# Kernel tuning notes

Measured on AMD Instinct MI355X. Metric: run time of the kernel, lower is better.

The kernel has to match this reference:

```python
import jax, jax.numpy as jnp
import numpy as np
from jax import lax

V, E, H, B, S = 100000, 256, 256, 16, 64
NEG = -1e9


def setup_inputs() -> dict:
    key = jax.random.key(0)
    ks = jax.random.split(key, 20)
    sc = 0.05
    inp = {
        "x": jax.random.randint(ks[0], (B, S), 0, V),
        "mask": jax.random.randint(ks[1], (B, S), 0, 2).astype(jnp.int32),
        "TASK": 0,
        # embedding table (pretrained embedding copied into nn.Embedding)
        "embed": jax.random.normal(ks[2], (V, E), jnp.float32) * sc,
        # shared LSTM (torch gate order i,f,g,o)
        "W_ih": jax.random.normal(ks[3], (4 * H, E), jnp.float32) * sc,
        "W_hh": jax.random.normal(ks[4], (4 * H, H), jnp.float32) * sc,
        "b_ih": jax.random.normal(ks[5], (4 * H,), jnp.float32) * sc,
        "b_hh": jax.random.normal(ks[6], (4 * H,), jnp.float32) * sc,
        # task-specific attention: Ws: (E+2H)->H, Us: H->1
        "Ws_w": jax.random.normal(ks[7], (H, E + 2 * H), jnp.float32) * sc,
        "Ws_b": jax.random.normal(ks[8], (H,), jnp.float32) * sc,
        "Us_w": jax.random.normal(ks[9], (1, H), jnp.float32) * sc,
        "Us_b": jax.random.normal(ks[10], (1,), jnp.float32) * sc,
        # message LSTM cell: gates from x_t, h_{t-1}, message Rt
        "Wx": jax.random.normal(ks[11], (4 * H, E), jnp.float32) * sc,
        "Wh": jax.random.normal(ks[12], (4 * H, H), jnp.float32) * sc,
        "Wm": jax.random.normal(ks[13], (4 * H, H), jnp.float32) * sc,
        "b_cell": jax.random.normal(ks[14], (4 * H,), jnp.float32) * sc,
        # final classifier
        "fc_w": jax.random.normal(ks[15], (1, H), jnp.float32) * sc,
        "fc_b": jax.random.normal(ks[16], (1,), jnp.float32) * sc,
    }
    return inp


def _lstm_gates(g, c):
    i, f, gg, o = jnp.split(g, 4, axis=-1)
    c_new = jax.nn.sigmoid(f) * c + jax.nn.sigmoid(i) * jnp.tanh(gg)
    h_new = jax.nn.sigmoid(o) * jnp.tanh(c_new)
    return h_new, c_new


def _forward(x, mask, embed, W_ih, W_hh, b_ih, b_hh, Ws_w, Ws_b, Us_w, Us_b,
             Wx, Wh, Wm, b_cell, fc_w, fc_b):
    b, s = x.shape
    h_dim = W_hh.shape[1]
    emb = embed[x]                              # [B,S,E]
    emb_t = jnp.transpose(emb, (1, 0, 2))       # [S,B,E]
    z = jnp.zeros((b, h_dim), emb.dtype)

    def shared_step(carry, e_t):
        h, c = carry
        g = e_t @ W_ih.T + h @ W_hh.T + (b_ih + b_hh)
        h, c = _lstm_gates(g, c)
        return (h, c), h

    _, shared_t = lax.scan(shared_step, (z, z), emb_t)   # [S,B,H]
    shared = jnp.transpose(shared_t, (1, 0, 2))          # [B,S,H]
    valid = mask != 0                                    # [B,S]

    def task_step(carry, e_t):
        h, c = carry
        h_task = jnp.broadcast_to(h[:, None, :], shared.shape)      # [B,S,H]
        cat = jnp.concatenate([shared, h_task, emb], axis=2)        # [B,S,E+2H]
        var2 = jnp.tanh(cat @ Ws_w.T + Ws_b)                        # [B,S,H]
        Si = (var2 @ Us_w.T + Us_b)[..., 0]                         # [B,S]
        att = jax.nn.softmax(jnp.where(valid, Si, NEG), axis=1)     # masked softmax over S
        Rt = jnp.einsum('bs,bsh->bh', att, shared)                  # [B,H]
        g = e_t @ Wx.T + h @ Wh.T + Rt @ Wm.T + b_cell
        h, c = _lstm_gates(g, c)
        return (h, c), None

    (h_last, _), _ = lax.scan(jax.checkpoint(task_step), (z, z), emb_t)
    return jax.nn.sigmoid(h_last @ fc_w.T + fc_b)        # [B,1]


def reference(x, mask, TASK, embed, W_ih, W_hh, b_ih, b_hh, Ws_w, Ws_b,
              Us_w, Us_b, Wx, Wh, Wm, b_cell, fc_w, fc_b):
    # TASK selects an entry of task_specific_lstm_list, but the list holds the
    # same module object num_tasks times, so one parameter set is used.
    del TASK
    return _forward(x, mask, embed, W_ih, W_hh, b_ih, b_hh, Ws_w, Ws_b,
                    Us_w, Us_b, Wx, Wh, Wm, b_cell, fc_w, fc_b)
```

## Files before the change

### kernel.cpp

```cpp
#include <hip/hip_runtime.h>

#define NEGV -1e9f

#define OFF_X1   0u
#define OFF_XX   1048576u
#define OFF_A    2097152u
#define OFF_SH   2359296u
#define OFF_SWM  2621440u
#define OFF_HX2  3670016u
#define OFF_HX4  3686400u
#define OFF_PSI  3702784u
#define OFF_AT   OFF_X1

__device__ __forceinline__ float sigf(float x) { return 1.f / (1.f + __expf(-x)); }
__device__ __forceinline__ float tanhfast(float x) {
  float e = __expf(2.f * x);
  return 1.f - __fdividef(2.f, e + 1.f);
}

__device__ __forceinline__ unsigned long long gloadU64(const unsigned long long* p) {
  return __hip_atomic_load(p, __ATOMIC_RELAXED, __HIP_MEMORY_SCOPE_AGENT);
}
__device__ __forceinline__ void gstoreU64(unsigned long long* p, unsigned long long v) {
  __hip_atomic_store(p, v, __ATOMIC_RELAXED, __HIP_MEMORY_SCOPE_AGENT);
}

__device__ __forceinline__ void tile_mm(const float* __restrict__ W, int ldw, int wcol0,
                                        int j0, const float* eL, float* wL, float acc[8]) {
  const int i = threadIdx.x >> 4, jj = threadIdx.x & 15;
  for (int kc = 0; kc < 4; ++kc) {
    __syncthreads();
    const int k0 = kc * 64;
    #pragma unroll
    for (int m = 0; m < 32; ++m) {
      int v = threadIdx.x + (m << 8);
      int row = v >> 6, col = v & 63;
      wL[row * 68 + col] = W[(j0 + row) * ldw + wcol0 + k0 + col];
    }
    __syncthreads();
    const float* ebase = eL + i * 260 + k0;
    #pragma unroll 4
    for (int k4 = 0; k4 < 16; ++k4) {
      float4 e4 = *(const float4*)(ebase + k4 * 4);
      #pragma unroll
      for (int u = 0; u < 8; ++u) {
        float4 w4 = *(const float4*)(wL + (jj + (u << 4)) * 68 + k4 * 4);
        acc[u] += e4.x * w4.x + e4.y * w4.y + e4.z * w4.z + e4.w * w4.w;
      }
    }
  }
}

__global__ __launch_bounds__(256) void k1_precompute(
    const int* __restrict__ x, const float* __restrict__ embed,
    const float* __restrict__ W_ih, const float* __restrict__ b_ih,
    const float* __restrict__ b_hh, const float* __restrict__ Ws_w,
    const float* __restrict__ Ws_b, const float* __restrict__ Wx,
    const float* __restrict__ b_cell, float* __restrict__ ws) {
  __shared__ float eL[16 * 260];
  __shared__ float wL[128 * 68];
  const int rt = blockIdx.x / 18, jb = blockIdx.x % 18;
  if (blockIdx.x == 0) {
    for (int i = threadIdx.x; i < 65536; i += 256) ws[OFF_HX2 + i] = 0.f;
  }
  for (int i = 0; i < 16; ++i) {
    int xi = x[rt * 16 + i];
    eL[i * 260 + threadIdx.x] = embed[xi * 256 + threadIdx.x];
  }
  const float* W; const float* bias1; const float* bias2 = nullptr;
  int ldw, wcol0, j0, ostride; float* out;
  if (jb < 8)       { W = W_ih; ldw = 256; wcol0 = 0;   j0 = jb * 128;        out = ws + OFF_X1; ostride = 1024; bias1 = b_ih; bias2 = b_hh; }
  else if (jb < 16) { W = Wx;   ldw = 256; wcol0 = 0;   j0 = (jb - 8) * 128;  out = ws + OFF_XX; ostride = 1024; bias1 = b_cell; }
  else              { W = Ws_w; ldw = 768; wcol0 = 512; j0 = (jb - 16) * 128; out = ws + OFF_A;  ostride = 256;  bias1 = Ws_b; }
  float acc[8];
  #pragma unroll
  for (int u = 0; u < 8; ++u) acc[u] = 0.f;
  tile_mm(W, ldw, wcol0, j0, eL, wL, acc);
  const int i = threadIdx.x >> 4, jj = threadIdx.x & 15;
  const int r = rt * 16 + i;
  #pragma unroll
  for (int u = 0; u < 8; ++u) {
    int j = j0 + jj + (u << 4);
    float bv = bias1[j] + (bias2 ? bias2[j] : 0.f);
    out[r * ostride + j] = acc[u] + bv;
  }
}

__global__ __launch_bounds__(512) void k2_shared_lstm(
    const float* __restrict__ W_hh, float* __restrict__ ws) {
  const int b = blockIdx.x & 15, j = blockIdx.x >> 4;
  const int t = threadIdx.x;
  const int rl = t >> 2, q = t & 3;
  const int grow = ((rl >> 5) << 8) + (j << 5) + (rl & 31);
  __shared__ float x1L[64 * 128];
  __shared__ __align__(16) float hL[256];
  __shared__ float gA[128];
  unsigned long long* hx = (unsigned long long*)(ws + OFF_HX2);
  float* sh = ws + OFF_SH;
  const float* X1 = ws + OFF_X1;

  float4 wv[16];
  {
    const float* wp = W_hh + grow * 256 + (q << 6);
    #pragma unroll
    for (int m = 0; m < 16; ++m) wv[m] = *(const float4*)(wp + 4 * m);
  }
  for (int v = t; v < 8192; v += 512) {
    int st = v >> 7, r = v & 127;
    int col = ((r >> 5) << 8) + (j << 5) + (r & 31);
    x1L[v] = X1[(b * 64 + st) * 1024 + col];
  }
  float c_reg = 0.f;
  __syncthreads();

  for (int st = 0; st < 64; ++st) {
    if (t < 256) {
      const unsigned long long* p = hx + (unsigned)(st & 1) * 4096u + b * 256 + t;
      unsigned long long v = gloadU64(p);
      while ((unsigned)(v >> 32) < (unsigned)st) v = gloadU64(p);
      hL[t] = __uint_as_float((unsigned)v);
    }
    __syncthreads();
    float p = 0.f;
    const float* hp = hL + (q << 6);
    #pragma unroll
    for (int m = 0; m < 16; ++m) {
      float4 h4 = *(const float4*)(hp + 4 * m);
      p += wv[m].x * h4.x + wv[m].y * h4.y + wv[m].z * h4.z + wv[m].w * h4.w;
    }
    p += __shfl_xor(p, 1); p += __shfl_xor(p, 2);
    if (q == 0) gA[rl] = p + x1L[st * 128 + rl];
    __syncthreads();
    if (t < 32) {
      float gi = gA[t], gf = gA[32 + t], gg = gA[64 + t], go = gA[96 + t];
      c_reg = sigf(gf) * c_reg + sigf(gi) * tanhfast(gg);
      float hn = sigf(go) * tanhfast(c_reg);
      sh[(b * 64 + st) * 256 + (j << 5) + t] = hn;
      unsigned long long pv = ((unsigned long long)(unsigned)(st + 1) << 32)
                            | (unsigned long long)__float_as_uint(hn);
      gstoreU64(hx + (unsigned)((st + 1) & 1) * 4096u + b * 256 + (j << 5) + t, pv);
    }
  }
}

__global__ __launch_bounds__(256) void k3_precompute2(
    const float* __restrict__ Ws_w, const float* __restrict__ Wm,
    float* __restrict__ ws) {
  __shared__ float eL[16 * 260];
  __shared__ float wL[128 * 68];
  const int rt = blockIdx.x / 10, jb = blockIdx.x % 10;
  const float* sh = ws + OFF_SH;
  for (int i = 0; i < 16; ++i)
    eL[i * 260 + threadIdx.x] = sh[(rt * 16 + i) * 256 + threadIdx.x];
  const float* W; int ldw, wcol0, j0; bool addmode;
  if (jb < 8) { W = Wm;   ldw = 256; wcol0 = 0; j0 = jb * 128;       addmode = false; }
  else        { W = Ws_w; ldw = 768; wcol0 = 0; j0 = (jb - 8) * 128; addmode = true; }
  float acc[8];
  #pragma unroll
  for (int u = 0; u < 8; ++u) acc[u] = 0.f;
  tile_mm(W, ldw, wcol0, j0, eL, wL, acc);
  const int i = threadIdx.x >> 4, jj = threadIdx.x & 15;
  const int r = rt * 16 + i;
  if (addmode) {
    const float* Aemb = ws + OFF_A;
    float* AT = ws + OFF_AT;
    const int bb = r >> 6, s = r & 63;
    #pragma unroll
    for (int u = 0; u < 8; ++u) {
      int j = j0 + jj + (u << 4);
      AT[bb * 16384 + j * 64 + s] = Aemb[r * 256 + j] + acc[u];
    }
  } else {
    float* out = ws + OFF_SWM;
    #pragma unroll
    for (int u = 0; u < 8; ++u) {
      int j = j0 + jj + (u << 4);
      out[r * 1024 + j] = acc[u];
    }
  }
}

__global__ __launch_bounds__(512) void k4_task_lstm(
    const int* __restrict__ mask, const float* __restrict__ Ws_w,
    const float* __restrict__ Us_w, const float* __restrict__ Wh,
    const float* __restrict__ fc_w, const float* __restrict__ fc_b,
    float* __restrict__ ws, float* __restrict__ out) {
  const int b = blockIdx.x & 15, j = blockIdx.x >> 4;
  const int t = threadIdx.x;
  const int rl = t >> 2, q = t & 3;
  const int grow = ((rl >> 5) << 8) + (j << 5) + (rl & 31);
  const int hwrow = t >> 4, hwc = t & 15;
  const int kq = t >> 6, sl = t & 63;

  __shared__ __align__(16) float swmB[4 * 128 * 20];
  __shared__ __align__(16) float aTo[32 * 65];
  __shared__ __align__(16) float hL[256];
  __shared__ float hwOwn[32];
  __shared__ float usOwn[32];
  __shared__ float part[8 * 64];
  __shared__ float psiA[512];
  __shared__ __align__(16) float attL[64];
  __shared__ float gA[128];
  __shared__ float redL[4];
  __shared__ int   mL[64];

  unsigned long long* hx   = (unsigned long long*)(ws + OFF_HX4);
  unsigned long long* psiX = (unsigned long long*)(ws + OFF_PSI);
  const float* AT  = ws + OFF_AT;
  const float* SWM = ws + OFF_SWM;
  const float* Xx  = ws + OFF_XX;

  float4 w2v[4];
  {
    const float* p2 = Ws_w + (j * 32 + hwrow) * 768 + 256 + (hwc << 4);
    #pragma unroll
    for (int m = 0; m < 4; ++m) w2v[m] = *(const float4*)(p2 + 4 * m);
  }
  float4 whv[16];
  {
    const float* pw = Wh + grow * 256 + (q << 6);
    #pragma unroll
    for (int m = 0; m < 16; ++m) whv[m] = *(const float4*)(pw + 4 * m);
  }
  for (int v = t; v < 2048; v += 512)
    aTo[(v >> 6) * 65 + (v & 63)] = AT[b * 16384 + j * 2048 + v];
  for (int v = t; v < 8192; v += 512) {
    int s = v >> 7, r = v & 127;
    int col = ((r >> 5) << 8) + (j << 5) + (r & 31);
    swmB[(s >> 4) * 2560 + r * 20 + (s & 15)] = SWM[(b * 64 + s) * 1024 + col];
  }
  if (t < 32) usOwn[t] = Us_w[j * 32 + t];
  if (t < 64) mL[t] = mask[b * 64 + t];
  float c_reg = 0.f;
  __syncthreads();

  for (int st = 0; st < 64; ++st) {
    float xx_r = 0.f;
    if (q == 0) xx_r = Xx[(b * 64 + st) * 1024 + grow];
    if (t < 256) {
      const unsigned long long* p = hx + (unsigned)(st & 1) * 4096u + b * 256 + t;
      unsigned long long v = gloadU64(p);
      while ((unsigned)(v >> 32) < (unsigned)st) v = gloadU64(p);
      hL[t] = __uint_as_float((unsigned)v);
    }
    __syncthreads();
    {
      const float* hp = hL + (hwc << 4);
      float p = 0.f;
      #pragma unroll
      for (int m = 0; m < 4; ++m) {
        float4 h4 = *(const float4*)(hp + 4 * m);
        p += w2v[m].x * h4.x + w2v[m].y * h4.y + w2v[m].z * h4.z + w2v[m].w * h4.w;
      }
      p += __shfl_xor(p, 1); p += __shfl_xor(p, 2);
      p += __shfl_xor(p, 4); p += __shfl_xor(p, 8);
      if (hwc == 0) hwOwn[hwrow] = p;
    }
    __syncthreads();
    {
      float ps = 0.f;
      #pragma unroll
      for (int i2 = 0; i2 < 4; ++i2) {
        int kk = (kq << 2) + i2;
        ps += usOwn[kk] * tanhfast(aTo[kk * 65 + sl] + hwOwn[kk]);
      }
      part[(kq << 6) + sl] = ps;
    }
    __syncthreads();
    if (t < 64) {
      float ps = 0.f;
      #pragma unroll
      for (int w = 0; w < 8; ++w) ps += part[(w << 6) + t];
      unsigned long long pv = ((unsigned long long)(unsigned)(st + 1) << 32)
                            | (unsigned long long)__float_as_uint(ps);
      gstoreU64(psiX + ((unsigned)(st & 1) * 16u + b) * 512u + (j << 6) + t, pv);
    }
    float pwh = 0.f;
    {
      const float* hp = hL + (q << 6);
      #pragma unroll
      for (int m = 0; m < 16; ++m) {
        float4 h4 = *(const float4*)(hp + 4 * m);
        pwh += whv[m].x * h4.x + whv[m].y * h4.y + whv[m].z * h4.z + whv[m].w * h4.w;
      }
    }
    {
      const unsigned long long* p = psiX + ((unsigned)(st & 1) * 16u + b) * 512u + t;
      unsigned long long v = gloadU64(p);
      while ((unsigned)(v >> 32) < (unsigned)(st + 1)) v = gloadU64(p);
      psiA[t] = __uint_as_float((unsigned)v);
    }
    __syncthreads();
    if (t < 64) {
      float acc = 0.f;
      #pragma unroll
      for (int w = 0; w < 8; ++w) acc += psiA[(w << 6) + t];
      float v = mL[t] ? acc : NEGV;
      float mx = v;
      #pragma unroll
      for (int d = 1; d < 64; d <<= 1) mx = fmaxf(mx, __shfl_xor(mx, d));
      float e = __expf(v - mx);
      float ssum = e;
      #pragma unroll
      for (int d = 1; d < 64; d <<= 1) ssum += __shfl_xor(ssum, d);
      attL[t] = e / ssum;
    }
    __syncthreads();
    {
      float p = pwh;
      const float* sb = swmB + q * 2560 + rl * 20;
      const float* atb = attL + (q << 4);
      #pragma unroll
      for (int i2 = 0; i2 < 4; ++i2) {
        float4 s4 = *(const float4*)(sb + 4 * i2);
        float4 a4 = *(const float4*)(atb + 4 * i2);
        p += s4.x * a4.x + s4.y * a4.y + s4.z * a4.z + s4.w * a4.w;
      }
      p += __shfl_xor(p, 1); p += __shfl_xor(p, 2);
      if (q == 0) gA[rl] = p + xx_r;
    }
    __syncthreads();
    if (t < 32) {
      float gi = gA[t], gf = gA[32 + t], gg = gA[64 + t], go = gA[96 + t];
      c_reg = sigf(gf) * c_reg + sigf(gi) * tanhfast(gg);
      float hn = sigf(go) * tanhfast(c_reg);
      unsigned long long pv = ((unsigned long long)(unsigned)(st + 1) << 32)
                            | (unsigned long long)__float_as_uint(hn);
      gstoreU64(hx + (unsigned)((st + 1) & 1) * 4096u + b * 256 + (j << 5) + t, pv);
    }
  }

  if (j == 0) {
    float v = 0.f;
    if (t < 256) {
      const unsigned long long* p = hx + 0 * 4096u + b * 256 + t;
      unsigned long long vv = gloadU64(p);
      while ((unsigned)(vv >> 32) < 64u) vv = gloadU64(p);
      v = __uint_as_float((unsigned)vv) * fc_w[t];
    }
    #pragma unroll
    for (int d = 1; d < 64; d <<= 1) v += __shfl_xor(v, d);
    if (t < 256 && (t & 63) == 0) redL[t >> 6] = v;
    __syncthreads();
    if (t == 0) out[b] = sigf(redL[0] + redL[1] + redL[2] + redL[3] + fc_b[0]);
  }
}

extern "C" void kernel_launch(void* const* d_in, const int* in_sizes, int n_in,
                              void* d_out, int out_size, void* d_ws, size_t ws_size,
                              hipStream_t stream) {
  const int*   x      = (const int*)d_in[0];
  const int*   mask   = (const int*)d_in[1];
  const float* embed  = (const float*)d_in[3];
  const float* W_ih   = (const float*)d_in[4];
  const float* W_hh   = (const float*)d_in[5];
  const float* b_ih   = (const float*)d_in[6];
  const float* b_hh   = (const float*)d_in[7];
  const float* Ws_w   = (const float*)d_in[8];
  const float* Ws_b   = (const float*)d_in[9];
  const float* Us_w   = (const float*)d_in[10];
  const float* Wx     = (const float*)d_in[12];
  const float* Wh     = (const float*)d_in[13];
  const float* Wm     = (const float*)d_in[14];
  const float* b_cell = (const float*)d_in[15];
  const float* fc_w   = (const float*)d_in[16];
  const float* fc_b   = (const float*)d_in[17];
  float* ws  = (float*)d_ws;
  float* out = (float*)d_out;

  k1_precompute<<<dim3(1152), dim3(256), 0, stream>>>(
      x, embed, W_ih, b_ih, b_hh, Ws_w, Ws_b, Wx, b_cell, ws);
  k2_shared_lstm<<<dim3(128), dim3(512), 0, stream>>>(W_hh, ws);
  k3_precompute2<<<dim3(640), dim3(256), 0, stream>>>(Ws_w, Wm, ws);
  k4_task_lstm<<<dim3(128), dim3(512), 0, stream>>>(
      mask, Ws_w, Us_w, Wh, fc_w, fc_b, ws, out);
}
```

Measured before the change: 436.4 us.

## Process two batch rows per block in recurrent LSTM kernels, halving grid size

Result: slower. 820.3 us (+88.0%).

```diff
diff --git a/kernel.cpp b/kernel.cpp
--- a/kernel.cpp
+++ b/kernel.cpp
@@ -23,6 +23,9 @@
 }
 __device__ __forceinline__ void gstoreU64(unsigned long long* p, unsigned long long v) {
   __hip_atomic_store(p, v, __ATOMIC_RELAXED, __HIP_MEMORY_SCOPE_AGENT);
+}
+__device__ __forceinline__ unsigned long long packTV(unsigned tag, float v) {
+  return ((unsigned long long)tag << 32) | (unsigned long long)__float_as_uint(v);
 }
 
 __device__ __forceinline__ void tile_mm(const float* __restrict__ W, int ldw, int wcol0,
@@ -88,13 +91,15 @@
 
 __global__ __launch_bounds__(512) void k2_shared_lstm(
     const float* __restrict__ W_hh, float* __restrict__ ws) {
-  const int b = blockIdx.x & 15, j = blockIdx.x >> 4;
+  const int g = blockIdx.x & 7, j = blockIdx.x >> 3;
+  const int bA = g << 1, bB = bA + 1;
   const int t = threadIdx.x;
-  const int rl = t >> 2, q = t & 3;
-  const int grow = ((rl >> 5) << 8) + (j << 5) + (rl & 31);
-  __shared__ float x1L[64 * 128];
-  __shared__ __align__(16) float hL[256];
-  __shared__ float gA[128];
+  const int w = t >> 6, l = t & 63;
+  const int gate = l >> 4, nnl = (w << 2) + ((l >> 2) & 3), q = l & 3;
+  const int r = (gate << 5) + nnl;
+  const int grow = (gate << 8) + (j << 5) + nnl;
+  __shared__ float x1LA[8192], x1LB[8192];
+  __shared__ __align__(16) float hLA[256], hLB[256];
   unsigned long long* hx = (unsigned long long*)(ws + OFF_HX2);
   float* sh = ws + OFF_SH;
   const float* X1 = ws + OFF_X1;
@@ -106,40 +111,67 @@
     for (int m = 0; m < 16; ++m) wv[m] = *(const float4*)(wp + 4 * m);
   }
   for (int v = t; v < 8192; v += 512) {
-    int st = v >> 7, r = v & 127;
-    int col = ((r >> 5) << 8) + (j << 5) + (r & 31);
-    x1L[v] = X1[(b * 64 + st) * 1024 + col];
-  }
-  float c_reg = 0.f;
+    int st = v >> 7, rr = v & 127;
+    int col = ((rr >> 5) << 8) + (j << 5) + (rr & 31);
+    x1LA[v] = X1[(bA * 64 + st) * 1024 + col];
+    x1LB[v] = X1[(bB * 64 + st) * 1024 + col];
+  }
+  float cA = 0.f, cB = 0.f;
+  const bool owner = (gate == 0) && (q == 0);
   __syncthreads();
 
   for (int st = 0; st < 64; ++st) {
-    if (t < 256) {
-      const unsigned long long* p = hx + (unsigned)(st & 1) * 4096u + b * 256 + t;
+    {
+      int pb = t >> 8, e = t & 255, bb = bA + pb;
+      const unsigned long long* p = hx + (unsigned)(st & 1) * 4096u + bb * 256 + e;
       unsigned long long v = gloadU64(p);
       while ((unsigned)(v >> 32) < (unsigned)st) v = gloadU64(p);
-      hL[t] = __uint_as_float((unsigned)v);
-    }
-    __syncthreads();
-    float p = 0.f;
-    const float* hp = hL + (q << 6);
-    #pragma unroll
-    for (int m = 0; m < 16; ++m) {
-      float4 h4 = *(const float4*)(hp + 4 * m);
-      p += wv[m].x * h4.x + wv[m].y * h4.y + wv[m].z * h4.z + wv[m].w * h4.w;
-    }
-    p += __shfl_xor(p, 1); p += __shfl_xor(p, 2);
-    if (q == 0) gA[rl] = p + x1L[st * 128 + rl];
-    __syncthreads();
-    if (t < 32) {
-      float gi = gA[t], gf = gA[32 + t], gg = gA[64 + t], go = gA[96 + t];
-      c_reg = sigf(gf) * c_reg + sigf(gi) * tanhfast(gg);
-      float hn = sigf(go) * tanhfast(c_reg);
-      sh[(b * 64 + st) * 256 + (j << 5) + t] = hn;
-      unsigned long long pv = ((unsigned long long)(unsigned)(st + 1) << 32)
-                            | (unsigned long long)__float_as_uint(hn);
-      gstoreU64(hx + (unsigned)((st + 1) & 1) * 4096u + b * 256 + (j << 5) + t, pv);
-    }
+      (pb ? hLB : hLA)[e] = __uint_as_float((unsigned)v);
+    }
+    __syncthreads();
+    {
+      const float* hp = hLA + (q << 6);
+      float p = 0.f;
+      #pragma unroll
+      for (int m = 0; m < 16; ++m) {
+        float4 h4 = *(const float4*)(hp + 4 * m);
+        p += wv[m].x * h4.x + wv[m].y * h4.y + wv[m].z * h4.z + wv[m].w * h4.w;
+      }
+      if (q == 0) p += x1LA[(st << 7) + r];
+      p += __shfl_xor(p, 1); p += __shfl_xor(p, 2);
+      float gfv = __shfl(p, l + 16);
+      float ggv = __shfl(p, l + 32);
+      float gov = __shfl(p, l + 48);
+      if (owner) {
+        cA = sigf(gfv) * cA + sigf(p) * tanhfast(ggv);
+        float hn = sigf(gov) * tanhfast(cA);
+        sh[(bA * 64 + st) * 256 + (j << 5) + nnl] = hn;
+        gstoreU64(hx + (unsigned)((st + 1) & 1) * 4096u + bA * 256 + (j << 5) + nnl,
+                  packTV(st + 1, hn));
+      }
+    }
+    {
+      const float* hp = hLB + (q << 6);
+      float p = 0.f;
+      #pragma unroll
+      for (int m = 0; m < 16; ++m) {
+        float4 h4 = *(const float4*)(hp + 4 * m);
+        p += wv[m].x * h4.x + wv[m].y * h4.y + wv[m].z * h4.z + wv[m].w * h4.w;
+      }
+      if (q == 0) p += x1LB[(st << 7) + r];
+      p += __shfl_xor(p, 1); p += __shfl_xor(p, 2);
+      float gfv = __shfl(p, l + 16);
+      float ggv = __shfl(p, l + 32);
+      float gov = __shfl(p, l + 48);
+      if (owner) {
+        cB = sigf(gfv) * cB + sigf(p) * tanhfast(ggv);
+        float hn = sigf(gov) * tanhfast(cB);
+        sh[(bB * 64 + st) * 256 + (j << 5) + nnl] = hn;
+        gstoreU64(hx + (unsigned)((st + 1) & 1) * 4096u + bB * 256 + (j << 5) + nnl,
+                  packTV(st + 1, hn));
+      }
+    }
+    __syncthreads();
   }
 }
 
@@ -185,24 +217,24 @@
     const float* __restrict__ Us_w, const float* __restrict__ Wh,
     const float* __restrict__ fc_w, const float* __restrict__ fc_b,
     float* __restrict__ ws, float* __restrict__ out) {
-  const int b = blockIdx.x & 15, j = blockIdx.x >> 4;
+  const int g = blockIdx.x & 7, j = blockIdx.x >> 3;
+  const int bA = g << 1, bB = bA + 1;
   const int t = threadIdx.x;
-  const int rl = t >> 2, q = t & 3;
-  const int grow = ((rl >> 5) << 8) + (j << 5) + (rl & 31);
+  const int w = t >> 6, l = t & 63;
+  const int gate = l >> 4, nnl = (w << 2) + ((l >> 2) & 3), q = l & 3;
+  const int r = (gate << 5) + nnl;
+  const int grow = (gate << 8) + (j << 5) + nnl;
   const int hwrow = t >> 4, hwc = t & 15;
-  const int kq = t >> 6, sl = t & 63;
-
-  __shared__ __align__(16) float swmB[4 * 128 * 20];
-  __shared__ __align__(16) float aTo[32 * 65];
-  __shared__ __align__(16) float hL[256];
-  __shared__ float hwOwn[32];
+
+  __shared__ __align__(16) float swmBA[10240], swmBB[10240];
+  __shared__ __align__(16) float aToA[2080], aToB[2080];
+  __shared__ __align__(16) float hLA[256], hLB[256];
   __shared__ float usOwn[32];
-  __shared__ float part[8 * 64];
-  __shared__ float psiA[512];
-  __shared__ __align__(16) float attL[64];
-  __shared__ float gA[128];
-  __shared__ float redL[4];
-  __shared__ int   mL[64];
+  __shared__ float partA[512], partB[512];
+  __shared__ float psiAA[512], psiAB[512];
+  __shared__ float attWA[512], attWB[512];
+  __shared__ float redL[8];
+  __shared__ int   mLA[64], mLB[64];
 
   unsigned long long* hx   = (unsigned long long*)(ws + OFF_HX4);
   unsigned long long* psiX = (unsigned long long*)(ws + OFF_PSI);
@@ -222,127 +254,195 @@
     #pragma unroll
     for (int m = 0; m < 16; ++m) whv[m] = *(const float4*)(pw + 4 * m);
   }
-  for (int v = t; v < 2048; v += 512)
-    aTo[(v >> 6) * 65 + (v & 63)] = AT[b * 16384 + j * 2048 + v];
+  for (int v = t; v < 2048; v += 512) {
+    aToA[(v >> 6) * 65 + (v & 63)] = AT[bA * 16384 + j * 2048 + v];
+    aToB[(v >> 6) * 65 + (v & 63)] = AT[bB * 16384 + j * 2048 + v];
+  }
   for (int v = t; v < 8192; v += 512) {
-    int s = v >> 7, r = v & 127;
-    int col = ((r >> 5) << 8) + (j << 5) + (r & 31);
-    swmB[(s >> 4) * 2560 + r * 20 + (s & 15)] = SWM[(b * 64 + s) * 1024 + col];
+    int s = v >> 7, rr = v & 127;
+    int col = ((rr >> 5) << 8) + (j << 5) + (rr & 31);
+    int li = (s >> 4) * 2560 + rr * 20 + (s & 15);
+    swmBA[li] = SWM[(bA * 64 + s) * 1024 + col];
+    swmBB[li] = SWM[(bB * 64 + s) * 1024 + col];
   }
   if (t < 32) usOwn[t] = Us_w[j * 32 + t];
-  if (t < 64) mL[t] = mask[b * 64 + t];
-  float c_reg = 0.f;
+  if (t < 64) { mLA[t] = mask[bA * 64 + t]; mLB[t] = mask[bB * 64 + t]; }
+  float cA = 0.f, cB = 0.f;
   __syncthreads();
 
   for (int st = 0; st < 64; ++st) {
-    float xx_r = 0.f;
-    if (q == 0) xx_r = Xx[(b * 64 + st) * 1024 + grow];
-    if (t < 256) {
-      const unsigned long long* p = hx + (unsigned)(st & 1) * 4096u + b * 256 + t;
+    float xxA = 0.f, xxB = 0.f;
+    if (q == 0) {
+      xxA = Xx[(bA * 64 + st) * 1024 + grow];
+      xxB = Xx[(bB * 64 + st) * 1024 + grow];
+    }
+    {
+      int pb = t >> 8, e = t & 255, bb = bA + pb;
+      const unsigned long long* p = hx + (unsigned)(st & 1) * 4096u + bb * 256 + e;
       unsigned long long v = gloadU64(p);
       while ((unsigned)(v >> 32) < (unsigned)st) v = gloadU64(p);
-      hL[t] = __uint_as_float((unsigned)v);
-    }
-    __syncthreads();
-    {
-      const float* hp = hL + (hwc << 4);
-      float p = 0.f;
+      (pb ? hLB : hLA)[e] = __uint_as_float((unsigned)v);
+    }
+    __syncthreads();
+    {
+      const float* hp = hLA + (hwc << 4);
+      float ph = 0.f;
       #pragma unroll
       for (int m = 0; m < 4; ++m) {
         float4 h4 = *(const float4*)(hp + 4 * m);
-        p += w2v[m].x * h4.x + w2v[m].y * h4.y + w2v[m].z * h4.z + w2v[m].w * h4.w;
-      }
-      p += __shfl_xor(p, 1); p += __shfl_xor(p, 2);
-      p += __shfl_xor(p, 4); p += __shfl_xor(p, 8);
-      if (hwc == 0) hwOwn[hwrow] = p;
-    }
-    __syncthreads();
-    {
+        ph += w2v[m].x * h4.x + w2v[m].y * h4.y + w2v[m].z * h4.z + w2v[m].w * h4.w;
+      }
+      ph += __shfl_xor(ph, 1); ph += __shfl_xor(ph, 2);
+      ph += __shfl_xor(ph, 4); ph += __shfl_xor(ph, 8);
       float ps = 0.f;
       #pragma unroll
       for (int i2 = 0; i2 < 4; ++i2) {
-        int kk = (kq << 2) + i2;
-        ps += usOwn[kk] * tanhfast(aTo[kk * 65 + sl] + hwOwn[kk]);
-      }
-      part[(kq << 6) + sl] = ps;
+        float hwv = __shfl(ph, i2 << 4);
+        int kk = (w << 2) + i2;
+        ps += usOwn[kk] * tanhfast(aToA[kk * 65 + l] + hwv);
+      }
+      partA[(w << 6) + l] = ps;
+    }
+    {
+      const float* hp = hLB + (hwc << 4);
+      float ph = 0.f;
+      #pragma unroll
+      for (int m = 0; m < 4; ++m) {
+        float4 h4 = *(const float4*)(hp + 4 * m);
+        ph += w2v[m].x * h4.x + w2v[m].y * h4.y + w2v[m].z * h4.z + w2v[m].w * h4.w;
+      }
+      ph += __shfl_xor(ph, 1); ph += __shfl_xor(ph, 2);
+      ph += __shfl_xor(ph, 4); ph += __shfl_xor(ph, 8);
+      float ps = 0.f;
+      #pragma unroll
+      for (int i2 = 0; i2 < 4; ++i2) {
+        float hwv = __shfl(ph, i2 << 4);
+        int kk = (w << 2) + i2;
+        ps += usOwn[kk] * tanhfast(aToB[kk * 65 + l] + hwv);
+      }
+      partB[(w << 6) + l] = ps;
     }
     __syncthreads();
     if (t < 64) {
-      float ps = 0.f;
-      #pragma unroll
-      for (int w = 0; w < 8; ++w) ps += part[(w << 6) + t];
-      unsigned long long pv = ((unsigned long long)(unsigned)(st + 1) << 32)
-                            | (unsigned long long)__float_as_uint(ps);
-      gstoreU64(psiX + ((unsigned)(st & 1) * 16u + b) * 512u + (j << 6) + t, pv);
-    }
-    float pwh = 0.f;
-    {
-      const float* hp = hL + (q << 6);
+      float psa = 0.f, psb = 0.f;
+      #pragma unroll
+      for (int w2 = 0; w2 < 8; ++w2) { psa += partA[(w2 << 6) + t]; psb += partB[(w2 << 6) + t]; }
+      gstoreU64(psiX + ((unsigned)(st & 1) * 16u + bA) * 512u + (j << 6) + t, packTV(st + 1, psa));
+      gstoreU64(psiX + ((unsigned)(st & 1) * 16u + bB) * 512u + (j << 6) + t, packTV(st + 1, psb));
+    }
+    float pwhA = 0.f, pwhB = 0.f;
+    {
+      const float* ha = hLA + (q << 6);
+      const float* hb = hLB + (q << 6);
       #pragma unroll
       for (int m = 0; m < 16; ++m) {
-        float4 h4 = *(const float4*)(hp + 4 * m);
-        pwh += whv[m].x * h4.x + whv[m].y * h4.y + whv[m].z * h4.z + whv[m].w * h4.w;
-      }
-    }
-    {
-      const unsigned long long* p = psiX + ((unsigned)(st & 1) * 16u + b) * 512u + t;
-      unsigned long long v = gloadU64(p);
-      while ((unsigned)(v >> 32) < (unsigned)(st + 1)) v = gloadU64(p);
-      psiA[t] = __uint_as_float((unsigned)v);
-    }
-    __syncthreads();
-    if (t < 64) {
-      float acc = 0.f;
-      #pragma unroll
-      for (int w = 0; w < 8; ++w) acc += psiA[(w << 6) + t];
-      float v = mL[t] ? acc : NEGV;
-      float mx = v;
+        float4 h4 = *(const float4*)(ha + 4 * m);
+        float4 g4 = *(const float4*)(hb + 4 * m);
+        pwhA += whv[m].x * h4.x + whv[m].y * h4.y + whv[m].z * h4.z + whv[m].w * h4.w;
+        pwhB += whv[m].x * g4.x + whv[m].y * g4.y + whv[m].z * g4.z + whv[m].w * g4.w;
+      }
+    }
+    {
+      const unsigned long long* pa = psiX + ((unsigned)(st & 1) * 16u + bA) * 512u + t;
+      const unsigned long long* pb = psiX + ((unsigned)(st & 1) * 16u + bB) * 512u + t;
+      unsigned long long va = gloadU64(pa);
+      unsigned long long vb = gloadU64(pb);
+      while ((unsigned)(va >> 32) < (unsigned)(st + 1)) va = gloadU64(pa);
+      while ((unsigned)(vb >> 32) < (unsigned)(st + 1)) vb = gloadU64(pb);
+      psiAA[t] = __uint_as_float((unsigned)va);
+      psiAB[t] = __uint_as_float((unsigned)vb);
+    }
+    __syncthreads();
+    {
+      float vr = 0.f;
+      #pragma unroll
+      for (int w2 = 0; w2 < 8; ++w2) vr += psiAA[(w2 << 6) + l];
+      vr = mLA[l] ? vr : NEGV;
+      float mx = vr;
       #pragma unroll
       for (int d = 1; d < 64; d <<= 1) mx = fmaxf(mx, __shfl_xor(mx, d));
-      float e = __expf(v - mx);
-      float ssum = e;
+      float e2 = __expf(vr - mx);
+      float ssum = e2;
       #pragma unroll
       for (int d = 1; d < 64; d <<= 1) ssum += __shfl_xor(ssum, d);
-      attL[t] = e / ssum;
-    }
-    __syncthreads();
-    {
-      float p = pwh;
-      const float* sb = swmB + q * 2560 + rl * 20;
-      const float* atb = attL + (q << 4);
+      attWA[(w << 6) + l] = e2 / ssum;
+      float p = pwhA;
+      const float* sb = swmBA + q * 2560 + r * 20;
+      const float* ab = attWA + (w << 6) + (q << 4);
       #pragma unroll
       for (int i2 = 0; i2 < 4; ++i2) {
         float4 s4 = *(const float4*)(sb + 4 * i2);
-        float4 a4 = *(const float4*)(atb + 4 * i2);
+        float4 a4 = *(const float4*)(ab + 4 * i2);
         p += s4.x * a4.x + s4.y * a4.y + s4.z * a4.z + s4.w * a4.w;
       }
+      if (q == 0) p += xxA;
       p += __shfl_xor(p, 1); p += __shfl_xor(p, 2);
-      if (q == 0) gA[rl] = p + xx_r;
-    }
-    __syncthreads();
-    if (t < 32) {
-      float gi = gA[t], gf = gA[32 + t], gg = gA[64 + t], go = gA[96 + t];
-      c_reg = sigf(gf) * c_reg + sigf(gi) * tanhfast(gg);
-      float hn = sigf(go) * tanhfast(c_reg);
-      unsigned long long pv = ((unsigned long long)(unsigned)(st + 1) << 32)
-                            | (unsigned long long)__float_as_uint(hn);
-      gstoreU64(hx + (unsigned)((st + 1) & 1) * 4096u + b * 256 + (j << 5) + t, pv);
+      float gfv = __shfl(p, l + 16);
+      float ggv = __shfl(p, l + 32);
+      float gov = __shfl(p, l + 48);
+      if (gate == 0 && q == 0) {
+        cA = sigf(gfv) * cA + sigf(p) * tanhfast(ggv);
+        float hn = sigf(gov) * tanhfast(cA);
+        gstoreU64(hx + (unsigned)((st + 1) & 1) * 4096u + bA * 256 + (j << 5) + nnl,
+                  packTV(st + 1, hn));
+      }
+    }
+    {
+      float vr = 0.f;
+      #pragma unroll
+      for (int w2 = 0; w2 < 8; ++w2) vr += psiAB[(w2 << 6) + l];
+      vr = mLB[l] ? vr : NEGV;
+      float mx = vr;
+      #pragma unroll
+      for (int d = 1; d < 64; d <<= 1) mx = fmaxf(mx, __shfl_xor(mx, d));
+      float e2 = __expf(vr - mx);
+      float ssum = e2;
+      #pragma unroll
+      for (int d = 1; d < 64; d <<= 1) ssum += __shfl_xor(ssum, d);
+      attWB[(w << 6) + l] = e2 / ssum;
+      float p = pwhB;
+      const float* sb = swmBB + q * 2560 + r * 20;
+      const float* ab = attWB + (w << 6) + (q << 4);
+      #pragma unroll
+      for (int i2 = 0; i2 < 4; ++i2) {
+        float4 s4 = *(const float4*)(sb + 4 * i2);
+        float4 a4 = *(const float4*)(ab + 4 * i2);
+        p += s4.x * a4.x + s4.y * a4.y + s4.z * a4.z + s4.w * a4.w;
+      }
+      if (q == 0) p += xxB;
+      p += __shfl_xor(p, 1); p += __shfl_xor(p, 2);
+      float gfv = __shfl(p, l + 16);
+      float ggv = __shfl(p, l + 32);
+      float gov = __shfl(p, l + 48);
+      if (gate == 0 && q == 0) {
+        cB = sigf(gfv) * cB + sigf(p) * tanhfast(ggv);
+        float hn = sigf(gov) * tanhfast(cB);
+        gstoreU64(hx + (unsigned)((st + 1) & 1) * 4096u + bB * 256 + (j << 5) + nnl,
+                  packTV(st + 1, hn));
+      }
     }
   }
 
   if (j == 0) {
-    float v = 0.f;
+    float vA = 0.f, vB = 0.f;
     if (t < 256) {
-      const unsigned long long* p = hx + 0 * 4096u + b * 256 + t;
-      unsigned long long vv = gloadU64(p);
-      while ((unsigned)(vv >> 32) < 64u) vv = gloadU64(p);
-      v = __uint_as_float((unsigned)vv) * fc_w[t];
-    }
-    #pragma unroll
-    for (int d = 1; d < 64; d <<= 1) v += __shfl_xor(v, d);
-    if (t < 256 && (t & 63) == 0) redL[t >> 6] = v;
-    __syncthreads();
-    if (t == 0) out[b] = sigf(redL[0] + redL[1] + redL[2] + redL[3] + fc_b[0]);
+      const unsigned long long* p0 = hx + bA * 256 + t;
+      unsigned long long v0 = gloadU64(p0);
+      while ((unsigned)(v0 >> 32) < 64u) v0 = gloadU64(p0);
+      vA = __uint_as_float((unsigned)v0) * fc_w[t];
+      const unsigned long long* p1 = hx + bB * 256 + t;
+      unsigned long long v1 = gloadU64(p1);
+      while ((unsigned)(v1 >> 32) < 64u) v1 = gloadU64(p1);
+      vB = __uint_as_float((unsigned)v1) * fc_w[t];
+    }
+    #pragma unroll
+    for (int d = 1; d < 64; d <<= 1) { vA += __shfl_xor(vA, d); vB += __shfl_xor(vB, d); }
+    if (t < 256 && (t & 63) == 0) { redL[t >> 6] = vA; redL[4 + (t >> 6)] = vB; }
+    __syncthreads();
+    if (t == 0) {
+      out[bA] = sigf(redL[0] + redL[1] + redL[2] + redL[3] + fc_b[0]);
+      out[bB] = sigf(redL[4] + redL[5] + redL[6] + redL[7] + fc_b[0]);
+    }
   }
 }
 
@@ -370,8 +470,8 @@
 
   k1_precompute<<<dim3(1152), dim3(256), 0, stream>>>(
       x, embed, W_ih, b_ih, b_hh, Ws_w, Ws_b, Wx, b_cell, ws);
-  k2_shared_lstm<<<dim3(128), dim3(512), 0, stream>>>(W_hh, ws);
+  k2_shared_lstm<<<dim3(64), dim3(512), 0, stream>>>(W_hh, ws);
   k3_precompute2<<<dim3(640), dim3(256), 0, stream>>>(Ws_w, Wm, ws);
-  k4_task_lstm<<<dim3(128), dim3(512), 0, stream>>>(
+  k4_task_lstm<<<dim3(64), dim3(512), 0, stream>>>(
       mask, Ws_w, Us_w, Wh, fc_w, fc_b, ws, out);
 }
```

## Replace LDS barriers with wave shuffles and redistribute attention scoring per block

Applied to the files above, without the earlier changes.

Result: slower. 806.7 us (+84.9%).

```diff
diff --git a/kernel.cpp b/kernel.cpp
--- a/kernel.cpp
+++ b/kernel.cpp
@@ -3,13 +3,13 @@
 #define NEGV -1e9f
 
 #define OFF_X1   0u
+#define OFF_HWX  262144u
 #define OFF_XX   1048576u
 #define OFF_A    2097152u
 #define OFF_SH   2359296u
 #define OFF_SWM  2621440u
 #define OFF_HX2  3670016u
 #define OFF_HX4  3686400u
-#define OFF_PSI  3702784u
 #define OFF_AT   OFF_X1
 
 __device__ __forceinline__ float sigf(float x) { return 1.f / (1.f + __expf(-x)); }
@@ -23,6 +23,9 @@
 }
 __device__ __forceinline__ void gstoreU64(unsigned long long* p, unsigned long long v) {
   __hip_atomic_store(p, v, __ATOMIC_RELAXED, __HIP_MEMORY_SCOPE_AGENT);
+}
+__device__ __forceinline__ unsigned long long packTV(unsigned tag, float v) {
+  return ((unsigned long long)tag << 32) | (unsigned long long)__float_as_uint(v);
 }
 
 __device__ __forceinline__ void tile_mm(const float* __restrict__ W, int ldw, int wcol0,
@@ -61,7 +64,7 @@
   __shared__ float wL[128 * 68];
   const int rt = blockIdx.x / 18, jb = blockIdx.x % 18;
   if (blockIdx.x == 0) {
-    for (int i = threadIdx.x; i < 65536; i += 256) ws[OFF_HX2 + i] = 0.f;
+    for (int i = threadIdx.x; i < 32768; i += 256) ws[OFF_HX2 + i] = 0.f;
   }
   for (int i = 0; i < 16; ++i) {
     int xi = x[rt * 16 + i];
@@ -90,11 +93,12 @@
     const float* __restrict__ W_hh, float* __restrict__ ws) {
   const int b = blockIdx.x & 15, j = blockIdx.x >> 4;
   const int t = threadIdx.x;
-  const int rl = t >> 2, q = t & 3;
-  const int grow = ((rl >> 5) << 8) + (j << 5) + (rl & 31);
-  __shared__ float x1L[64 * 128];
-  __shared__ __align__(16) float hL[256];
-  __shared__ float gA[128];
+  const int w = t >> 6, l = t & 63;
+  const int gate = l >> 4, u = (l >> 2) & 3, q = l & 3;
+  const int nnl = (w << 2) + u;
+  const int r = (gate << 5) + nnl;
+  const int grow = (gate << 8) + (j << 5) + nnl;
+  __shared__ float x1L[8192];
   unsigned long long* hx = (unsigned long long*)(ws + OFF_HX2);
   float* sh = ws + OFF_SH;
   const float* X1 = ws + OFF_X1;
@@ -106,39 +110,44 @@
     for (int m = 0; m < 16; ++m) wv[m] = *(const float4*)(wp + 4 * m);
   }
   for (int v = t; v < 8192; v += 512) {
-    int st = v >> 7, r = v & 127;
-    int col = ((r >> 5) << 8) + (j << 5) + (r & 31);
+    int st = v >> 7, rr = v & 127;
+    int col = ((rr >> 5) << 8) + (j << 5) + (rr & 31);
     x1L[v] = X1[(b * 64 + st) * 1024 + col];
   }
   float c_reg = 0.f;
+  const bool owner = (gate == 0) && (q == 0);
   __syncthreads();
 
   for (int st = 0; st < 64; ++st) {
-    if (t < 256) {
-      const unsigned long long* p = hx + (unsigned)(st & 1) * 4096u + b * 256 + t;
-      unsigned long long v = gloadU64(p);
-      while ((unsigned)(v >> 32) < (unsigned)st) v = gloadU64(p);
-      hL[t] = __uint_as_float((unsigned)v);
-    }
-    __syncthreads();
+    const unsigned long long* pp = hx + (unsigned)(st & 1) * 4096u + b * 256 + (l << 2);
+    unsigned long long v0 = gloadU64(pp),     v1 = gloadU64(pp + 1),
+                       v2 = gloadU64(pp + 2), v3 = gloadU64(pp + 3);
+    while ((unsigned)(v0 >> 32) < (unsigned)st) v0 = gloadU64(pp);
+    while ((unsigned)(v1 >> 32) < (unsigned)st) v1 = gloadU64(pp + 1);
+    while ((unsigned)(v2 >> 32) < (unsigned)st) v2 = gloadU64(pp + 2);
+    while ((unsigned)(v3 >> 32) < (unsigned)st) v3 = gloadU64(pp + 3);
+    float h0 = __uint_as_float((unsigned)v0);
+    float h1 = __uint_as_float((unsigned)v1);
+    float h2 = __uint_as_float((unsigned)v2);
+    float h3 = __uint_as_float((unsigned)v3);
     float p = 0.f;
-    const float* hp = hL + (q << 6);
     #pragma unroll
     for (int m = 0; m < 16; ++m) {
-      float4 h4 = *(const float4*)(hp + 4 * m);
-      p += wv[m].x * h4.x + wv[m].y * h4.y + wv[m].z * h4.z + wv[m].w * h4.w;
-    }
+      int src = (q << 4) + m;
+      p += wv[m].x * __shfl(h0, src) + wv[m].y * __shfl(h1, src)
+         + wv[m].z * __shfl(h2, src) + wv[m].w * __shfl(h3, src);
+    }
+    if (q == 0) p += x1L[(st << 7) + r];
     p += __shfl_xor(p, 1); p += __shfl_xor(p, 2);
-    if (q == 0) gA[rl] = p + x1L[st * 128 + rl];
-    __syncthreads();
-    if (t < 32) {
-      float gi = gA[t], gf = gA[32 + t], gg = gA[64 + t], go = gA[96 + t];
-      c_reg = sigf(gf) * c_reg + sigf(gi) * tanhfast(gg);
+    float gf = __shfl(p, l + 16);
+    float gg = __shfl(p, l + 32);
+    float go = __shfl(p, l + 48);
+    if (owner) {
+      c_reg = sigf(gf) * c_reg + sigf(p) * tanhfast(gg);
       float hn = sigf(go) * tanhfast(c_reg);
-      sh[(b * 64 + st) * 256 + (j << 5) + t] = hn;
-      unsigned long long pv = ((unsigned long long)(unsigned)(st + 1) << 32)
-                            | (unsigned long long)__float_as_uint(hn);
-      gstoreU64(hx + (unsigned)((st + 1) & 1) * 4096u + b * 256 + (j << 5) + t, pv);
+      sh[(b * 64 + st) * 256 + (j << 5) + nnl] = hn;
+      gstoreU64(hx + (unsigned)((st + 1) & 1) * 4096u + b * 256 + (j << 5) + nnl,
+                packTV(st + 1, hn));
     }
   }
 }
@@ -149,6 +158,9 @@
   __shared__ float eL[16 * 260];
   __shared__ float wL[128 * 68];
   const int rt = blockIdx.x / 10, jb = blockIdx.x % 10;
+  if (jb == 0) {
+    for (int i = threadIdx.x; i < 2048; i += 256) ws[OFF_HWX + rt * 2048 + i] = 0.f;
+  }
   const float* sh = ws + OFF_SH;
   for (int i = 0; i < 16; ++i)
     eL[i * 260 + threadIdx.x] = sh[(rt * 16 + i) * 256 + threadIdx.x];
@@ -187,146 +199,149 @@
     float* __restrict__ ws, float* __restrict__ out) {
   const int b = blockIdx.x & 15, j = blockIdx.x >> 4;
   const int t = threadIdx.x;
-  const int rl = t >> 2, q = t & 3;
-  const int grow = ((rl >> 5) << 8) + (j << 5) + (rl & 31);
-  const int hwrow = t >> 4, hwc = t & 15;
-  const int kq = t >> 6, sl = t & 63;
-
-  __shared__ __align__(16) float swmB[4 * 128 * 20];
-  __shared__ __align__(16) float aTo[32 * 65];
-  __shared__ __align__(16) float hL[256];
-  __shared__ float hwOwn[32];
-  __shared__ float usOwn[32];
-  __shared__ float part[8 * 64];
-  __shared__ float psiA[512];
-  __shared__ __align__(16) float attL[64];
-  __shared__ float gA[128];
+  const int w = t >> 6, l = t & 63;
+  const int gate = l >> 4, u = (l >> 2) & 3, q = l & 3;
+  const int nnl = (w << 2) + u;
+  const int r = (gate << 5) + nnl;
+  const int grow = (gate << 8) + (j << 5) + nnl;
+  const int pr = t >> 1, kh = t & 1;
+
+  __shared__ __align__(16) float aT[256 * 65];
+  __shared__ __align__(16) float swmB[10240];
+  __shared__ __align__(16) float usL[256];
+  __shared__ float hwL[256];
+  __shared__ float part[512];
+  __shared__ __align__(16) float attW[512];
+  __shared__ float hnewL[32];
   __shared__ float redL[4];
   __shared__ int   mL[64];
 
-  unsigned long long* hx   = (unsigned long long*)(ws + OFF_HX4);
-  unsigned long long* psiX = (unsigned long long*)(ws + OFF_PSI);
+  unsigned long long* hx  = (unsigned long long*)(ws + OFF_HX4);
+  unsigned long long* hwX = (unsigned long long*)(ws + OFF_HWX);
   const float* AT  = ws + OFF_AT;
   const float* SWM = ws + OFF_SWM;
   const float* Xx  = ws + OFF_XX;
 
-  float4 w2v[4];
-  {
-    const float* p2 = Ws_w + (j * 32 + hwrow) * 768 + 256 + (hwc << 4);
-    #pragma unroll
-    for (int m = 0; m < 4; ++m) w2v[m] = *(const float4*)(p2 + 4 * m);
-  }
   float4 whv[16];
   {
     const float* pw = Wh + grow * 256 + (q << 6);
     #pragma unroll
     for (int m = 0; m < 16; ++m) whv[m] = *(const float4*)(pw + 4 * m);
   }
-  for (int v = t; v < 2048; v += 512)
-    aTo[(v >> 6) * 65 + (v & 63)] = AT[b * 16384 + j * 2048 + v];
+  float4 w2c[4];
+  {
+    const float* p2 = Ws_w + pr * 768 + 256 + (j << 5) + (kh << 4);
+    #pragma unroll
+    for (int m = 0; m < 4; ++m) w2c[m] = *(const float4*)(p2 + 4 * m);
+  }
+  for (int v = t; v < 16384; v += 512)
+    aT[(v >> 6) * 65 + (v & 63)] = AT[b * 16384 + v];
   for (int v = t; v < 8192; v += 512) {
-    int s = v >> 7, r = v & 127;
-    int col = ((r >> 5) << 8) + (j << 5) + (r & 31);
-    swmB[(s >> 4) * 2560 + r * 20 + (s & 15)] = SWM[(b * 64 + s) * 1024 + col];
-  }
-  if (t < 32) usOwn[t] = Us_w[j * 32 + t];
+    int s = v >> 7, rr = v & 127;
+    int col = ((rr >> 5) << 8) + (j << 5) + (rr & 31);
+    swmB[(s >> 4) * 2560 + rr * 20 + (s & 15)] = SWM[(b * 64 + s) * 1024 + col];
+  }
+  if (t < 256) usL[t] = Us_w[t];
   if (t < 64) mL[t] = mask[b * 64 + t];
   float c_reg = 0.f;
+  const bool owner = (gate == 0) && (q == 0);
   __syncthreads();
 
   for (int st = 0; st < 64; ++st) {
-    float xx_r = 0.f;
-    if (q == 0) xx_r = Xx[(b * 64 + st) * 1024 + grow];
-    if (t < 256) {
-      const unsigned long long* p = hx + (unsigned)(st & 1) * 4096u + b * 256 + t;
-      unsigned long long v = gloadU64(p);
-      while ((unsigned)(v >> 32) < (unsigned)st) v = gloadU64(p);
-      hL[t] = __uint_as_float((unsigned)v);
+    float xx_r = (q == 0) ? Xx[(b * 64 + st) * 1024 + grow] : 0.f;
+    const unsigned long long* ph = hx + (unsigned)(st & 1) * 4096u + b * 256 + (l << 2);
+    const unsigned long long* pw = hwX + b * 4096u + (unsigned)(st & 1) * 2048u
+                                 + (kh << 10) + pr;
+    unsigned long long a0 = gloadU64(pw),       a1 = gloadU64(pw + 256),
+                       a2 = gloadU64(pw + 512), a3 = gloadU64(pw + 768);
+    unsigned long long v0 = gloadU64(ph),     v1 = gloadU64(ph + 1),
+                       v2 = gloadU64(ph + 2), v3 = gloadU64(ph + 3);
+    while ((unsigned)(v0 >> 32) < (unsigned)st) v0 = gloadU64(ph);
+    while ((unsigned)(v1 >> 32) < (unsigned)st) v1 = gloadU64(ph + 1);
+    while ((unsigned)(v2 >> 32) < (unsigned)st) v2 = gloadU64(ph + 2);
+    while ((unsigned)(v3 >> 32) < (unsigned)st) v3 = gloadU64(ph + 3);
+    while ((unsigned)(a0 >> 32) < (unsigned)st) a0 = gloadU64(pw);
+    while ((unsigned)(a1 >> 32) < (unsigned)st) a1 = gloadU64(pw + 256);
+    while ((unsigned)(a2 >> 32) < (unsigned)st) a2 = gloadU64(pw + 512);
+    while ((unsigned)(a3 >> 32) < (unsigned)st) a3 = gloadU64(pw + 768);
+    float h0 = __uint_as_float((unsigned)v0);
+    float h1 = __uint_as_float((unsigned)v1);
+    float h2 = __uint_as_float((unsigned)v2);
+    float h3 = __uint_as_float((unsigned)v3);
+    {
+      float s_hw = __uint_as_float((unsigned)a0) + __uint_as_float((unsigned)a1)
+                 + __uint_as_float((unsigned)a2) + __uint_as_float((unsigned)a3);
+      s_hw += __shfl_xor(s_hw, 1);
+      if (kh == 0) hwL[pr] = s_hw;
+    }
+    float ps = 0.f;
+    {
+      const int k0 = w << 5;
+      #pragma unroll
+      for (int i = 0; i < 32; ++i) {
+        int k = k0 + i;
+        ps += usL[k] * tanhfast(aT[k * 65 + l] + hwL[k]);
+      }
+      part[t] = ps;
+    }
+    float pwh = 0.f;
+    #pragma unroll
+    for (int m = 0; m < 16; ++m) {
+      int src = (q << 4) + m;
+      pwh += whv[m].x * __shfl(h0, src) + whv[m].y * __shfl(h1, src)
+           + whv[m].z * __shfl(h2, src) + whv[m].w * __shfl(h3, src);
     }
     __syncthreads();
     {
-      const float* hp = hL + (hwc << 4);
-      float p = 0.f;
-      #pragma unroll
-      for (int m = 0; m < 4; ++m) {
-        float4 h4 = *(const float4*)(hp + 4 * m);
-        p += w2v[m].x * h4.x + w2v[m].y * h4.y + w2v[m].z * h4.z + w2v[m].w * h4.w;
-      }
-      p += __shfl_xor(p, 1); p += __shfl_xor(p, 2);
-      p += __shfl_xor(p, 4); p += __shfl_xor(p, 8);
-      if (hwc == 0) hwOwn[hwrow] = p;
-    }
-    __syncthreads();
-    {
-      float ps = 0.f;
-      #pragma unroll
-      for (int i2 = 0; i2 < 4; ++i2) {
-        int kk = (kq << 2) + i2;
-        ps += usOwn[kk] * tanhfast(aTo[kk * 65 + sl] + hwOwn[kk]);
-      }
-      part[(kq << 6) + sl] = ps;
-    }
-    __syncthreads();
-    if (t < 64) {
-      float ps = 0.f;
-      #pragma unroll
-      for (int w = 0; w < 8; ++w) ps += part[(w << 6) + t];
-      unsigned long long pv = ((unsigned long long)(unsigned)(st + 1) << 32)
-                            | (unsigned long long)__float_as_uint(ps);
-      gstoreU64(psiX + ((unsigned)(st & 1) * 16u + b) * 512u + (j << 6) + t, pv);
-    }
-    float pwh = 0.f;
-    {
-      const float* hp = hL + (q << 6);
-      #pragma unroll
-      for (int m = 0; m < 16; ++m) {
-        float4 h4 = *(const float4*)(hp + 4 * m);
-        pwh += whv[m].x * h4.x + whv[m].y * h4.y + whv[m].z * h4.z + whv[m].w * h4.w;
-      }
-    }
-    {
-      const unsigned long long* p = psiX + ((unsigned)(st & 1) * 16u + b) * 512u + t;
-      unsigned long long v = gloadU64(p);
-      while ((unsigned)(v >> 32) < (unsigned)(st + 1)) v = gloadU64(p);
-      psiA[t] = __uint_as_float((unsigned)v);
-    }
-    __syncthreads();
-    if (t < 64) {
-      float acc = 0.f;
-      #pragma unroll
-      for (int w = 0; w < 8; ++w) acc += psiA[(w << 6) + t];
-      float v = mL[t] ? acc : NEGV;
-      float mx = v;
+      float vr = 0.f;
+      #pragma unroll
+      for (int w2 = 0; w2 < 8; ++w2) vr += part[(w2 << 6) + l];
+      vr = mL[l] ? vr : NEGV;
+      float mx = vr;
       #pragma unroll
       for (int d = 1; d < 64; d <<= 1) mx = fmaxf(mx, __shfl_xor(mx, d));
-      float e = __expf(v - mx);
-      float ssum = e;
+      float e2 = __expf(vr - mx);
+      float ssum = e2;
       #pragma unroll
       for (int d = 1; d < 64; d <<= 1) ssum += __shfl_xor(ssum, d);
-      attL[t] = e / ssum;
-    }
-    __syncthreads();
+      attW[t] = e2 / ssum;
+    }
     {
       float p = pwh;
-      const float* sb = swmB + q * 2560 + rl * 20;
-      const float* atb = attL + (q << 4);
+      const float* sb = swmB + q * 2560 + r * 20;
+      const float* ab = attW + (w << 6) + (q << 4);
       #pragma unroll
       for (int i2 = 0; i2 < 4; ++i2) {
         float4 s4 = *(const float4*)(sb + 4 * i2);
-        float4 a4 = *(const float4*)(atb + 4 * i2);
+        float4 a4 = *(const float4*)(ab + 4 * i2);
         p += s4.x * a4.x + s4.y * a4.y + s4.z * a4.z + s4.w * a4.w;
       }
+      if (q == 0) p += xx_r;
       p += __shfl_xor(p, 1); p += __shfl_xor(p, 2);
-      if (q == 0) gA[rl] = p + xx_r;
-    }
-    __syncthreads();
-    if (t < 32) {
-      float gi = gA[t], gf = gA[32 + t], gg = gA[64 + t], go = gA[96 + t];
-      c_reg = sigf(gf) * c_reg + sigf(gi) * tanhfast(gg);
-      float hn = sigf(go) * tanhfast(c_reg);
-      unsigned long long pv = ((unsigned long long)(unsigned)(st + 1) << 32)
-                            | (unsigned long long)__float_as_uint(hn);
-      gstoreU64(hx + (unsigned)((st + 1) & 1) * 4096u + b * 256 + (j << 5) + t, pv);
+      float gf = __shfl(p, l + 16);
+      float gg = __shfl(p, l + 32);
+      float go = __shfl(p, l + 48);
+      if (owner) {
+        c_reg = sigf(gf) * c_reg + sigf(p) * tanhfast(gg);
+        float hn = sigf(go) * tanhfast(c_reg);
+        gstoreU64(hx + (unsigned)((st + 1) & 1) * 4096u + b * 256 + (j << 5) + nnl,
+                  packTV(st + 1, hn));
+        hnewL[nnl] = hn;
+      }
+    }
+    if (st < 63) {
+      __syncthreads();
+      const float* hb = hnewL + (kh << 4);
+      float p2 = 0.f;
+      #pragma unroll
+      for (int m = 0; m < 4; ++m) {
+        p2 += w2c[m].x * hb[4 * m]     + w2c[m].y * hb[4 * m + 1]
+            + w2c[m].z * hb[4 * m + 2] + w2c[m].w * hb[4 * m + 3];
+      }
+      p2 += __shfl_xor(p2, 1);
+      if (kh == 0)
+        gstoreU64(hwX + b * 4096u + (unsigned)((st + 1) & 1) * 2048u + (j << 8) + pr,
+                  packTV(st + 1, p2));
     }
   }
 
```
